# Optimization experiments

Hardware: AMD Instinct MI355X
Metric: run time of the kernel (lower is better)

The kernel has to match this reference:

```python
import jax, jax.numpy as jnp
import numpy as np

B, L, H = 32, 4096, 512

def setup_inputs() -> dict:
    key = jax.random.key(0)
    k1, k2, k3, k4 = jax.random.split(key, 4)
    output = jax.random.normal(k1, (B, H), dtype=jnp.float32)
    context = jax.random.normal(k2, (B, L, H), dtype=jnp.float32)
    # nn.Linear(2H, H): weight [H, 2H], bias [H]
    W = jax.random.normal(k3, (H, 2 * H), dtype=jnp.float32) / np.sqrt(2 * H)
    b = jax.random.normal(k4, (H,), dtype=jnp.float32) * 0.01
    return {"output": output, "context": context, "W": W, "b": b}

def reference(output, context, W, b):
    # output: [B, H] single-step query; context: [B, L, H]
    scores = jnp.einsum('bh,blh->bl', output, context)          # [B, L]
    # original masks exact zeros to -inf before softmax
    scores = jnp.where(scores == 0, -jnp.inf, scores)
    attn = jax.nn.softmax(scores, axis=-1)                      # [B, L]
    # rows that were all -inf produce NaN -> set to 0 (faithful to nan_mask fill)
    attn = jnp.where(jnp.isnan(attn), 0.0, attn)
    mix = jnp.einsum('bl,blh->bh', attn, context)               # [B, H]
    combined = jnp.concatenate([mix, output], axis=-1)          # [B, 2H]
    out = jnp.tanh(combined @ W.T + b)                          # [B, H]
    return out, attn[:, None, :]                                # attn: [B, 1, L]
```

## Files before the change

### kernel.cpp

```cpp
#include <hip/hip_runtime.h>
#include <math.h>

#define B_SZ 32
#define L_SZ 4096
#define H_SZ 512
#define S_SPLIT 32
#define CHUNK (L_SZ / S_SPLIT)
#define ROWS_PER_WAVE (CHUNK / 4)

__global__ __launch_bounds__(256, 4)
void attn_pass1(const float* __restrict__ q,
                const float* __restrict__ ctx,
                float* __restrict__ scores_out,
                float* __restrict__ m_part,
                float* __restrict__ s_part,
                float* __restrict__ acc_part)
{
    const int bid   = blockIdx.x;
    const int b     = bid / S_SPLIT;
    const int split = bid % S_SPLIT;
    const int tid   = threadIdx.x;
    const int wave  = tid >> 6;
    const int lane  = tid & 63;

    const float4* qv = (const float4*)(q + (size_t)b * H_SZ);
    const float4 q0 = qv[lane];
    const float4 q1 = qv[64 + lane];

    float  m = -INFINITY;
    float  s = 0.f;
    float4 a0 = make_float4(0.f, 0.f, 0.f, 0.f);
    float4 a1 = make_float4(0.f, 0.f, 0.f, 0.f);

    float my_scores[ROWS_PER_WAVE / 64 + 1];
    float sc_keep = 0.f;

    const int l0 = split * CHUNK + wave * ROWS_PER_WAVE;
    const float* ctx_b = ctx + (size_t)b * L_SZ * H_SZ;
    (void)my_scores;

    #pragma unroll 2
    for (int i = 0; i < ROWS_PER_WAVE; ++i) {
        const int l = l0 + i;
        const float4* cv = (const float4*)(ctx_b + (size_t)l * H_SZ);
        const float4 c0 = cv[lane];
        const float4 c1 = cv[64 + lane];

        float p = q0.x*c0.x + q0.y*c0.y + q0.z*c0.z + q0.w*c0.w
                + q1.x*c1.x + q1.y*c1.y + q1.z*c1.z + q1.w*c1.w;
        #pragma unroll
        for (int off = 32; off >= 1; off >>= 1)
            p += __shfl_xor(p, off, 64);
        const float sc = p;

        if (lane == i) sc_keep = sc;

        if (sc != 0.0f) {
            const float m_new = fmaxf(m, sc);
            const float corr  = __expf(m - m_new);
            const float pw    = __expf(sc - m_new);
            s = s * corr + pw;
            a0.x = a0.x * corr + pw * c0.x;
            a0.y = a0.y * corr + pw * c0.y;
            a0.z = a0.z * corr + pw * c0.z;
            a0.w = a0.w * corr + pw * c0.w;
            a1.x = a1.x * corr + pw * c1.x;
            a1.y = a1.y * corr + pw * c1.y;
            a1.z = a1.z * corr + pw * c1.z;
            a1.w = a1.w * corr + pw * c1.w;
            m = m_new;
        }
    }

    if (lane < ROWS_PER_WAVE)
        scores_out[(size_t)b * L_SZ + l0 + lane] = sc_keep;

    __shared__ float lds_m[4];
    __shared__ float lds_s[4];
    __shared__ float lds_acc[4][H_SZ];
    if (lane == 0) { lds_m[wave] = m; lds_s[wave] = s; }
    float* la = lds_acc[wave];
    *(float4*)(la + 4 * lane)       = a0;
    *(float4*)(la + 256 + 4 * lane) = a1;
    __syncthreads();

    const float mb = fmaxf(fmaxf(lds_m[0], lds_m[1]), fmaxf(lds_m[2], lds_m[3]));
    float sb = 0.f, ac0 = 0.f, ac1 = 0.f;
    #pragma unroll
    for (int w = 0; w < 4; ++w) {
        const float wg = (lds_s[w] > 0.f) ? __expf(lds_m[w] - mb) : 0.f;
        sb  += wg * lds_s[w];
        ac0 += wg * lds_acc[w][tid];
        ac1 += wg * lds_acc[w][tid + 256];
    }
    const int ps = b * S_SPLIT + split;
    if (tid == 0) { m_part[ps] = mb; s_part[ps] = sb; }
    acc_part[(size_t)ps * H_SZ + tid]       = ac0;
    acc_part[(size_t)ps * H_SZ + tid + 256] = ac1;
}

__global__ __launch_bounds__(256)
void attn_pass2(const float* __restrict__ q,
                const float* __restrict__ W,
                const float* __restrict__ bias,
                const float* __restrict__ m_part,
                const float* __restrict__ s_part,
                const float* __restrict__ acc_part,
                float* __restrict__ out,
                float* __restrict__ attn)
{
    const int b   = blockIdx.x;
    const int tid = threadIdx.x;

    __shared__ float mix_s[H_SZ];
    __shared__ float q_s[H_SZ];

    float m = -INFINITY;
    #pragma unroll
    for (int j = 0; j < S_SPLIT; ++j)
        m = fmaxf(m, m_part[b * S_SPLIT + j]);

    float stot = 0.f, mx0 = 0.f, mx1 = 0.f;
    #pragma unroll
    for (int j = 0; j < S_SPLIT; ++j) {
        const float sj = s_part[b * S_SPLIT + j];
        const float wg = (sj > 0.f) ? __expf(m_part[b * S_SPLIT + j] - m) : 0.f;
        stot += wg * sj;
        const float* ap = acc_part + (size_t)(b * S_SPLIT + j) * H_SZ;
        mx0 += wg * ap[tid];
        mx1 += wg * ap[tid + 256];
    }
    const float inv = (stot > 0.f) ? 1.f / stot : 0.f;
    mix_s[tid]       = mx0 * inv;
    mix_s[tid + 256] = mx1 * inv;
    q_s[tid]         = q[(size_t)b * H_SZ + tid];
    q_s[tid + 256]   = q[(size_t)b * H_SZ + tid + 256];

    for (int l = tid; l < L_SZ; l += 256) {
        const float sc = attn[(size_t)b * L_SZ + l];
        const float a  = (sc != 0.0f) ? __expf(sc - m) * inv : 0.f;
        attn[(size_t)b * L_SZ + l] = a;
    }
    __syncthreads();

    const int h0 = tid;
    const int h1 = tid + 256;
    const float4* w0 = (const float4*)(W + (size_t)h0 * (2 * H_SZ));
    const float4* w1 = (const float4*)(W + (size_t)h1 * (2 * H_SZ));
    const float4* mixv = (const float4*)mix_s;
    const float4* qv   = (const float4*)q_s;

    float acc0 = bias[h0];
    float acc1 = bias[h1];
    #pragma unroll 4
    for (int k = 0; k < H_SZ / 4; ++k) {
        const float4 mv = mixv[k];
        const float4 a  = w0[k];
        const float4 c  = w1[k];
        acc0 += a.x*mv.x + a.y*mv.y + a.z*mv.z + a.w*mv.w;
        acc1 += c.x*mv.x + c.y*mv.y + c.z*mv.z + c.w*mv.w;
    }
    #pragma unroll 4
    for (int k = 0; k < H_SZ / 4; ++k) {
        const float4 qq = qv[k];
        const float4 a  = w0[H_SZ / 4 + k];
        const float4 c  = w1[H_SZ / 4 + k];
        acc0 += a.x*qq.x + a.y*qq.y + a.z*qq.z + a.w*qq.w;
        acc1 += c.x*qq.x + c.y*qq.y + c.z*qq.z + c.w*qq.w;
    }
    out[(size_t)b * H_SZ + h0] = tanhf(acc0);
    out[(size_t)b * H_SZ + h1] = tanhf(acc1);
}

extern "C" void kernel_launch(void* const* d_in, const int* in_sizes, int n_in,
                              void* d_out, int out_size, void* d_ws, size_t ws_size,
                              hipStream_t stream) {
    const float* q    = (const float*)d_in[0];
    const float* ctx  = (const float*)d_in[1];
    const float* W    = (const float*)d_in[2];
    const float* bias = (const float*)d_in[3];

    float* out  = (float*)d_out;
    float* attn = out + B_SZ * H_SZ;

    float* ws       = (float*)d_ws;
    float* m_part   = ws;
    float* s_part   = ws + B_SZ * S_SPLIT;
    float* acc_part = ws + 2 * B_SZ * S_SPLIT;

    attn_pass1<<<B_SZ * S_SPLIT, 256, 0, stream>>>(q, ctx, attn, m_part, s_part, acc_part);
    attn_pass2<<<B_SZ, 256, 0, stream>>>(q, W, bias, m_part, s_part, acc_part, out, attn);
}
```

Measured before the change: 437.7 us.

## Split combine and output GEMV into separate kernels with wave-per-output GEMV

Replaces the single 32-block epilogue kernel with a 512-thread combine kernel that writes the mix vector and normalizes attention, plus a GEMV kernel where each wave computes one output element with coalesced row reads of W. This targets the low parallelism and strided W access of the old epilogue. It adds one extra kernel launch and a workspace round-trip for the mix vector.

```diff
diff --git a/kernel.cpp b/kernel.cpp
--- a/kernel.cpp
+++ b/kernel.cpp
@@ -32,12 +32,10 @@
     float4 a0 = make_float4(0.f, 0.f, 0.f, 0.f);
     float4 a1 = make_float4(0.f, 0.f, 0.f, 0.f);
 
-    float my_scores[ROWS_PER_WAVE / 64 + 1];
     float sc_keep = 0.f;
 
     const int l0 = split * CHUNK + wave * ROWS_PER_WAVE;
     const float* ctx_b = ctx + (size_t)b * L_SZ * H_SZ;
-    (void)my_scores;
 
     #pragma unroll 2
     for (int i = 0; i < ROWS_PER_WAVE; ++i) {
@@ -99,77 +97,75 @@
     acc_part[(size_t)ps * H_SZ + tid + 256] = ac1;
 }
 
-__global__ __launch_bounds__(256)
-void attn_pass2(const float* __restrict__ q,
-                const float* __restrict__ W,
-                const float* __restrict__ bias,
-                const float* __restrict__ m_part,
-                const float* __restrict__ s_part,
-                const float* __restrict__ acc_part,
-                float* __restrict__ out,
-                float* __restrict__ attn)
+__global__ __launch_bounds__(512)
+void attn_combine(const float* __restrict__ m_part,
+                  const float* __restrict__ s_part,
+                  const float* __restrict__ acc_part,
+                  float* __restrict__ mix_out,
+                  float* __restrict__ attn)
 {
     const int b   = blockIdx.x;
     const int tid = threadIdx.x;
-
-    __shared__ float mix_s[H_SZ];
-    __shared__ float q_s[H_SZ];
 
     float m = -INFINITY;
     #pragma unroll
     for (int j = 0; j < S_SPLIT; ++j)
         m = fmaxf(m, m_part[b * S_SPLIT + j]);
 
-    float stot = 0.f, mx0 = 0.f, mx1 = 0.f;
+    float stot = 0.f, mx = 0.f;
     #pragma unroll
     for (int j = 0; j < S_SPLIT; ++j) {
         const float sj = s_part[b * S_SPLIT + j];
         const float wg = (sj > 0.f) ? __expf(m_part[b * S_SPLIT + j] - m) : 0.f;
         stot += wg * sj;
-        const float* ap = acc_part + (size_t)(b * S_SPLIT + j) * H_SZ;
-        mx0 += wg * ap[tid];
-        mx1 += wg * ap[tid + 256];
+        mx   += wg * acc_part[(size_t)(b * S_SPLIT + j) * H_SZ + tid];
     }
     const float inv = (stot > 0.f) ? 1.f / stot : 0.f;
-    mix_s[tid]       = mx0 * inv;
-    mix_s[tid + 256] = mx1 * inv;
-    q_s[tid]         = q[(size_t)b * H_SZ + tid];
-    q_s[tid + 256]   = q[(size_t)b * H_SZ + tid + 256];
+    mix_out[(size_t)b * H_SZ + tid] = mx * inv;
 
-    for (int l = tid; l < L_SZ; l += 256) {
+    #pragma unroll
+    for (int l = tid; l < L_SZ; l += 512) {
         const float sc = attn[(size_t)b * L_SZ + l];
-        const float a  = (sc != 0.0f) ? __expf(sc - m) * inv : 0.f;
-        attn[(size_t)b * L_SZ + l] = a;
+        attn[(size_t)b * L_SZ + l] = (sc != 0.0f) ? __expf(sc - m) * inv : 0.f;
     }
-    __syncthreads();
+}
 
-    const int h0 = tid;
-    const int h1 = tid + 256;
-    const float4* w0 = (const float4*)(W + (size_t)h0 * (2 * H_SZ));
-    const float4* w1 = (const float4*)(W + (size_t)h1 * (2 * H_SZ));
-    const float4* mixv = (const float4*)mix_s;
-    const float4* qv   = (const float4*)q_s;
+__global__ __launch_bounds__(256)
+void attn_gemv(const float* __restrict__ q,
+               const float* __restrict__ W,
+               const float* __restrict__ bias,
+               const float* __restrict__ mix,
+               float* __restrict__ out)
+{
+    const int wave = threadIdx.x >> 6;
+    const int lane = threadIdx.x & 63;
+    const int oi   = blockIdx.x * 4 + wave;
+    const int b    = oi >> 9;
+    const int h    = oi & (H_SZ - 1);
 
-    float acc0 = bias[h0];
-    float acc1 = bias[h1];
-    #pragma unroll 4
-    for (int k = 0; k < H_SZ / 4; ++k) {
-        const float4 mv = mixv[k];
-        const float4 a  = w0[k];
-        const float4 c  = w1[k];
-        acc0 += a.x*mv.x + a.y*mv.y + a.z*mv.z + a.w*mv.w;
-        acc1 += c.x*mv.x + c.y*mv.y + c.z*mv.z + c.w*mv.w;
-    }
-    #pragma unroll 4
-    for (int k = 0; k < H_SZ / 4; ++k) {
-        const float4 qq = qv[k];
-        const float4 a  = w0[H_SZ / 4 + k];
-        const float4 c  = w1[H_SZ / 4 + k];
-        acc0 += a.x*qq.x + a.y*qq.y + a.z*qq.z + a.w*qq.w;
-        acc1 += c.x*qq.x + c.y*qq.y + c.z*qq.z + c.w*qq.w;
-    }
-    out[(size_t)b * H_SZ + h0] = tanhf(acc0);
-    out[(size_t)b * H_SZ + h1] = tanhf(acc1);
+    const float4* Wr = (const float4*)(W + (size_t)h * (2 * H_SZ));
+    const float4* mv = (const float4*)(mix + (size_t)b * H_SZ);
+    const float4* qv = (const float4*)(q   + (size_t)b * H_SZ);
+
+    const float4 w0 = Wr[lane];
+    const float4 w1 = Wr[64 + lane];
+    const float4 w2 = Wr[128 + lane];
+    const float4 w3 = Wr[192 + lane];
+    const float4 x0 = mv[lane];
+    const float4 x1 = mv[64 + lane];
+    const float4 y0 = qv[lane];
+    const float4 y1 = qv[64 + lane];
+
+    float p = w0.x*x0.x + w0.y*x0.y + w0.z*x0.z + w0.w*x0.w
+            + w1.x*x1.x + w1.y*x1.y + w1.z*x1.z + w1.w*x1.w
+            + w2.x*y0.x + w2.y*y0.y + w2.z*y0.z + w2.w*y0.w
+            + w3.x*y1.x + w3.y*y1.y + w3.z*y1.z + w3.w*y1.w;
+    #pragma unroll
+    for (int off = 32; off >= 1; off >>= 1)
+        p += __shfl_xor(p, off, 64);
+
+    if (lane == 0)
+        out[oi] = tanhf(p + bias[h]);
 }
 
 extern "C" void kernel_launch(void* const* d_in, const int* in_sizes, int n_in,
@@ -187,7 +183,9 @@
     float* m_part   = ws;
     float* s_part   = ws + B_SZ * S_SPLIT;
     float* acc_part = ws + 2 * B_SZ * S_SPLIT;
+    float* mix      = acc_part + (size_t)B_SZ * S_SPLIT * H_SZ;
 
     attn_pass1<<<B_SZ * S_SPLIT, 256, 0, stream>>>(q, ctx, attn, m_part, s_part, acc_part);
-    attn_pass2<<<B_SZ, 256, 0, stream>>>(q, W, bias, m_part, s_part, acc_part, out, attn);
+    attn_combine<<<B_SZ, 512, 0, stream>>>(m_part, s_part, acc_part, mix, attn);
+    attn_gemv<<<(B_SZ * H_SZ) / 4, 256, 0, stream>>>(q, W, bias, mix, out);
 }
```

Result: faster. 375.8 us (-14.2%).
